# Kernel optimization log

Hardware: AMD Instinct MI355X
Metric: run time of the kernel (lower is better)

The kernel has to match this reference:

```python
import jax, jax.numpy as jnp
import numpy as np

H_IMG, W_IMG = 48, 64  # feature-map resolution hard-coded in the module
NUM_HEADS = 8


def get_positional_encodings(B, N, dtype=jnp.float32):
    # (p3^2, p4^2, p3*p4, p3, p4, 1) on normalized grid; intrinsics=None path
    ys = jnp.linspace(-1.0, 1.0, H_IMG, dtype=dtype)
    xs = jnp.linspace(-1.0, 1.0, W_IMG, dtype=dtype)
    p3 = jnp.tile(ys, W_IMG)           # [N] = ys repeated W times (torch repeat)
    p4 = jnp.repeat(xs, H_IMG)         # [N] = each x repeated H times
    pos = jnp.stack([p3 * p3, p4 * p4, p3 * p4, p3, p4, jnp.ones_like(p3)], axis=-1)  # [N,6]
    return jnp.broadcast_to(pos[None], (B, N, 6))


def setup_inputs() -> dict:
    key = jax.random.key(0)
    k1, k2, k3, k4, k5 = jax.random.split(key, 5)
    B, N, C = 2, H_IMG * W_IMG, 256
    s = 0.02
    return {
        "x1": jax.random.normal(k1, (B, N, C), jnp.float32),
        "x2": jax.random.normal(k2, (B, N, C), jnp.float32),
        "Wq": jax.random.normal(k3, (C, C), jnp.float32) * s,      # qkv (one-way: q only)
        "Wkv": jax.random.normal(k4, (C, 2 * C), jnp.float32) * s,  # qkv2 -> k,v
        "Wpf": jax.random.normal(k5, (C + 6 * NUM_HEADS, C), jnp.float32) * s,  # proj_fundamental
        "bpf": jnp.zeros((C,), jnp.float32),
    }


def reference(x1, x2, Wq, Wkv, Wpf, bpf):
    B, N, C = x1.shape
    H = NUM_HEADS
    d = C // H
    scale = d ** -0.5

    # q from x1; k,v from x2 (separate linear, matching torch reshape/permute split)
    q1 = (x1 @ Wq).reshape(B, N, H, d).transpose(0, 2, 1, 3)          # [B,H,N,d]
    kv = (x2 @ Wkv).reshape(B, N, 2, H, d)
    k2 = kv[:, :, 0].transpose(0, 2, 1, 3)                            # [B,H,N,d]
    v2 = kv[:, :, 1].transpose(0, 2, 1, 3)                            # [B,H,N,d]

    attn = jax.nn.softmax(jnp.einsum('bhnd,bhmd->bhnm', q1, k2) * scale, axis=-1)  # [B,H,N,N]

    pos = get_positional_encodings(B, N, x1.dtype)                    # [B,N,6]
    v2p = jnp.concatenate(
        [v2, jnp.broadcast_to(pos[:, None], (B, H, N, 6))], axis=-1)  # [B,H,N,d+6]

    y = jnp.einsum('bhnm,bhmd->bhnd', attn, v2p)                      # [B,H,N,d+6]
    y = y.transpose(0, 2, 1, 3).reshape(B, N, H * (d + 6))            # [B,N,C+6H]
    y = y @ Wpf + bpf                                                 # [B,N,C]
    y = y.reshape(B, N, H, d).transpose(0, 2, 1, 3)                   # [B,H,N,d]

    return jnp.concatenate([attn, y], axis=-1)                        # [B,H,N,N+d]
```

## Files before the change

### kernel.cpp

```cpp
#include <hip/hip_runtime.h>
#include <hip/hip_bf16.h>
#include <cstdint>
#include <cstddef>

#define NB 2
#define NH 8
#define BHN 16
#define NN 3072
#define CC 256
#define DD 32
#define OUTW 3104
#define VW 48
#define KP 384

typedef __attribute__((ext_vector_type(8))) __bf16 bf16x8;
typedef __attribute__((ext_vector_type(4))) short short4v;
typedef __attribute__((ext_vector_type(4))) float f32x4;

static __device__ __forceinline__ unsigned short f2bf(float f) {
    __hip_bfloat16 h = __float2bfloat16(f);
    return *reinterpret_cast<unsigned short*>(&h);
}

static __device__ __forceinline__ bf16x8 ldb8(const unsigned short* p) {
    return *(const bf16x8*)p;
}

static __device__ __forceinline__ f32x4 mfma16(bf16x8 a, bf16x8 b, f32x4 c) {
    return __builtin_amdgcn_mfma_f32_16x16x32_bf16(a, b, c, 0, 0, 0);
}

static __device__ __forceinline__ float bfhi2f(unsigned u) {
    union { unsigned u; float f; } v; v.u = u & 0xffff0000u; return v.f;
}
static __device__ __forceinline__ float bflo2f(unsigned u) {
    union { unsigned u; float f; } v; v.u = u << 16; return v.f;
}

__global__ __launch_bounds__(256) void prep_kernel(
    const float* __restrict__ x1, const float* __restrict__ x2,
    const float* __restrict__ Wq, const float* __restrict__ Wkv,
    const float* __restrict__ Wpf,
    unsigned short* __restrict__ x1b, unsigned short* __restrict__ x2b,
    unsigned short* __restrict__ Wt, unsigned short* __restrict__ Wpft,
    unsigned short* __restrict__ v2pT)
{
    int i = blockIdx.x * 256 + threadIdx.x;
    const int S_X = NB * NN * CC;
    if (i < S_X) { x1b[i] = f2bf(x1[i]); return; }
    i -= S_X;
    if (i < S_X) { x2b[i] = f2bf(x2[i]); return; }
    i -= S_X;
    const int S_WT = 768 * CC;
    if (i < S_WT) {
        int j = i >> 8, kk = i & 255;
        float w = (j < 256) ? Wq[kk * 256 + j] : Wkv[kk * 512 + (j - 256)];
        Wt[i] = f2bf(w);
        return;
    }
    i -= S_WT;
    const int S_WP = 256 * KP;
    if (i < S_WP) {
        int c2 = i / KP, t = i - c2 * KP;
        int h = t / VW, cc = t - h * VW;
        unsigned short v = 0;
        if (cc < 38) v = f2bf(Wpf[(h * 38 + cc) * 256 + c2]);
        Wpft[i] = v;
        return;
    }
    i -= S_WP;
    const int S_POS = BHN * 16 * NN;
    if (i < S_POS) {
        int n = i % NN;
        int r = i / NN;
        int bh = r >> 4;
        int c = (r & 15) + 32;
        float val = 0.f;
        if (c < 38) {
            float p3 = -1.f + 2.f * (float)(n % 48) / 47.f;
            float p4 = -1.f + 2.f * (float)(n / 48) / 63.f;
            float pv[6] = { p3 * p3, p4 * p4, p3 * p4, p3, p4, 1.f };
            val = pv[c - 32];
        }
        v2pT[((size_t)bh * VW + c) * NN + n] = f2bf(val);
    }
}

__global__ __launch_bounds__(256) void qkv_kernel(
    const unsigned short* __restrict__ x1b, const unsigned short* __restrict__ x2b,
    const unsigned short* __restrict__ Wt,
    unsigned short* __restrict__ qbh, unsigned short* __restrict__ kbh,
    unsigned short* __restrict__ v2pT)
{
    int rt = blockIdx.x, ct = blockIdx.y;
    int wv = threadIdx.x >> 6, lane = threadIdx.x & 63;
    int g = lane >> 4, q = lane & 15;
    int row0 = rt * 64 + wv * 16;
    const unsigned short* A = (ct < 4) ? x1b : x2b;
    const unsigned short* arow = A + (size_t)(row0 + q) * CC + g * 8;
    const unsigned short* brow = Wt + (size_t)(ct * 64 + q) * CC + g * 8;
    f32x4 acc[4];
    #pragma unroll
    for (int cb = 0; cb < 4; ++cb) acc[cb] = f32x4{0.f, 0.f, 0.f, 0.f};
    for (int k0 = 0; k0 < CC; k0 += 32) {
        bf16x8 af = ldb8(arow + k0);
        #pragma unroll
        for (int cb = 0; cb < 4; ++cb)
            acc[cb] = mfma16(af, ldb8(brow + (size_t)cb * 16 * CC + k0), acc[cb]);
    }
    int b = row0 / NN, nb = row0 % NN;
    #pragma unroll
    for (int cb = 0; cb < 4; ++cb) {
        int jj = ct * 64 + cb * 16 + q;
        #pragma unroll
        for (int r = 0; r < 4; ++r) {
            int n = nb + 4 * g + r;
            unsigned short bv = f2bf(acc[cb][r]);
            if (jj < 256) {
                int h = jj >> 5, c = jj & 31;
                qbh[(size_t)((b * NH + h) * NN + n) * DD + c] = bv;
            } else if (jj < 512) {
                int jk = jj - 256; int h = jk >> 5, c = jk & 31;
                kbh[(size_t)((b * NH + h) * NN + n) * DD + c] = bv;
            } else {
                int jv = jj - 512; int h = jv >> 5, c = jv & 31;
                v2pT[(size_t)((b * NH + h) * VW + c) * NN + n] = bv;
            }
        }
    }
}

__global__ __launch_bounds__(256) void attn_kernel(
    const unsigned short* __restrict__ qbh, const unsigned short* __restrict__ kbh,
    const unsigned short* __restrict__ v2pT,
    float* __restrict__ out, unsigned short* __restrict__ yacc)
{
    __shared__ unsigned short ptile[4][16][256];
    const float C = 0.17677669529663687f * 1.4426950408889634f;

    int id = blockIdx.x;
    int xcd = id & 7;
    int slot = id >> 3;
    int bh = xcd * 2 + (slot & 1);
    int qt = slot >> 1;

    int wv = threadIdx.x >> 6, lane = threadIdx.x & 63;
    int g = lane >> 4, q = lane & 15;
    int qrow = qt * 64 + wv * 16;

    bf16x8 qf = ldb8(qbh + (size_t)(bh * NN + qrow + q) * DD + g * 8);
    const unsigned short* kbase = kbh + (size_t)bh * NN * DD;
    const unsigned short* vbase = v2pT + (size_t)bh * VW * NN;

    float l = 0.f;
    {
        bf16x8 kf0 = ldb8(kbase + (size_t)(q) * DD + g * 8);
        bf16x8 kf1 = ldb8(kbase + (size_t)(16 + q) * DD + g * 8);
        for (int it = 0; it < 96; ++it) {
            int m0 = it * 32;
            bf16x8 kn0 = ldb8(kbase + (size_t)(m0 + 32 + q) * DD + g * 8);
            bf16x8 kn1 = ldb8(kbase + (size_t)(m0 + 48 + q) * DD + g * 8);
            f32x4 z = {0.f, 0.f, 0.f, 0.f};
            f32x4 s0 = mfma16(kf0, qf, z);
            f32x4 s1 = mfma16(kf1, qf, z);
            #pragma unroll
            for (int r = 0; r < 4; ++r)
                l += exp2f(s0[r] * C) + exp2f(s1[r] * C);
            kf0 = kn0; kf1 = kn1;
        }
    }
    l += __shfl_xor(l, 16, 64);
    l += __shfl_xor(l, 32, 64);
    float nl2 = -__log2f(l);

    f32x4 yt0 = {0.f,0.f,0.f,0.f}, yt1 = yt0, yt2 = yt0;
    char* myt = (char*)&ptile[wv][0][0];
    char* prow = myt + q * 512;
    unsigned swq = (unsigned)((q & 7) << 4);

    bf16x8 kf0 = ldb8(kbase + (size_t)(q) * DD + g * 8);
    bf16x8 kf1 = ldb8(kbase + (size_t)(16 + q) * DD + g * 8);
    bf16x8 vf0 = ldb8(vbase + (size_t)(q) * NN + g * 8);
    bf16x8 vf1 = ldb8(vbase + (size_t)(16 + q) * NN + g * 8);
    bf16x8 vf2 = ldb8(vbase + (size_t)(32 + q) * NN + g * 8);

    for (int ph = 0; ph < 12; ++ph) {
        #pragma unroll
        for (int it2 = 0; it2 < 8; ++it2) {
            int m0 = ph * 256 + it2 * 32;
            bf16x8 kn0 = ldb8(kbase + (size_t)(m0 + 32 + q) * DD + g * 8);
            bf16x8 kn1 = ldb8(kbase + (size_t)(m0 + 48 + q) * DD + g * 8);
            bf16x8 vn0 = ldb8(vbase + (size_t)(q) * NN + m0 + 32 + g * 8);
            bf16x8 vn1 = ldb8(vbase + (size_t)(16 + q) * NN + m0 + 32 + g * 8);
            bf16x8 vn2 = ldb8(vbase + (size_t)(32 + q) * NN + m0 + 32 + g * 8);

            f32x4 z = {0.f, 0.f, 0.f, 0.f};
            f32x4 s0 = mfma16(kf0, qf, z);
            f32x4 s1 = mfma16(kf1, qf, z);
            short4v pk0, pk1;
            #pragma unroll
            for (int r = 0; r < 4; ++r) {
                pk0[r] = (short)f2bf(exp2f(__builtin_fmaf(s0[r], C, nl2)));
                pk1[r] = (short)f2bf(exp2f(__builtin_fmaf(s1[r], C, nl2)));
            }
            unsigned b0 = (unsigned)(it2 * 64 + 8 * g);
            *(short4v*)(prow + (b0 ^ swq)) = pk0;
            *(short4v*)(prow + ((b0 + 32) ^ swq)) = pk1;
            asm volatile("s_waitcnt lgkmcnt(0)" ::: "memory");
            __builtin_amdgcn_sched_barrier(0);
            bf16x8 pf = *(const bf16x8*)(prow + ((unsigned)(it2 * 64 + 16 * g) ^ swq));
            yt0 = mfma16(vf0, pf, yt0);
            yt1 = mfma16(vf1, pf, yt1);
            yt2 = mfma16(vf2, pf, yt2);
            kf0 = kn0; kf1 = kn1; vf0 = vn0; vf1 = vn1; vf2 = vn2;
        }
        #pragma unroll
        for (int i = 0; i < 16; ++i) {
            unsigned off = ((unsigned)(lane * 8)) ^ ((unsigned)((i & 7) << 4));
            uint2 d = *(const uint2*)(myt + i * 512 + off);
            f32x4 v;
            v[0] = bflo2f(d.x); v[1] = bfhi2f(d.x);
            v[2] = bflo2f(d.y); v[3] = bfhi2f(d.y);
            float* dst = out + (size_t)(bh * NN + qrow + i) * OUTW + ph * 256 + lane * 4;
            *(f32x4*)dst = v;
        }
    }

    int b = bh >> 3, h = bh & 7;
    int nrow = qrow + q;
    unsigned short* yrow = yacc + (size_t)(b * NN + nrow) * KP + h * VW;
    f32x4 yts[3] = { yt0, yt1, yt2 };
    #pragma unroll
    for (int cb = 0; cb < 3; ++cb) {
        short4v pk;
        #pragma unroll
        for (int r = 0; r < 4; ++r) pk[r] = (short)f2bf(yts[cb][r]);
        *(short4v*)(yrow + cb * 16 + 4 * g) = pk;
    }
}

__global__ __launch_bounds__(256) void proj_kernel(
    const unsigned short* __restrict__ yacc, const unsigned short* __restrict__ Wpft,
    const float* __restrict__ bpf, float* __restrict__ out)
{
    int rt = blockIdx.x, ct = blockIdx.y;
    int wv = threadIdx.x >> 6, lane = threadIdx.x & 63;
    int g = lane >> 4, q = lane & 15;
    int row0 = rt * 64 + wv * 16;
    const unsigned short* arow = yacc + (size_t)(row0 + q) * KP + g * 8;
    const unsigned short* b0 = Wpft + (size_t)(ct * 64 + q) * KP + g * 8;
    f32x4 acc[4];
    #pragma unroll
    for (int cb = 0; cb < 4; ++cb) acc[cb] = f32x4{0.f, 0.f, 0.f, 0.f};
    for (int k0 = 0; k0 < KP; k0 += 32) {
        bf16x8 af = ldb8(arow + k0);
        #pragma unroll
        for (int cb = 0; cb < 4; ++cb)
            acc[cb] = mfma16(af, ldb8(b0 + (size_t)cb * 16 * KP + k0), acc[cb]);
    }
    int b = row0 / NN, nb = row0 % NN;
    #pragma unroll
    for (int cb = 0; cb < 4; ++cb) {
        int c2 = ct * 64 + cb * 16 + q;
        float bias = bpf[c2];
        int h = c2 >> 5, c = c2 & 31;
        float* obase = out + (size_t)((b * NH + h) * NN) * OUTW + NN + c;
        #pragma unroll
        for (int r = 0; r < 4; ++r) {
            int n = nb + 4 * g + r;
            __builtin_nontemporal_store(acc[cb][r] + bias, &obase[(size_t)n * OUTW]);
        }
    }
}

extern "C" void kernel_launch(void* const* d_in, const int* in_sizes, int n_in,
                              void* d_out, int out_size, void* d_ws, size_t ws_size,
                              hipStream_t stream)
{
    (void)in_sizes; (void)n_in; (void)out_size; (void)ws_size;
    const float* x1  = (const float*)d_in[0];
    const float* x2  = (const float*)d_in[1];
    const float* Wq  = (const float*)d_in[2];
    const float* Wkv = (const float*)d_in[3];
    const float* Wpf = (const float*)d_in[4];
    const float* bpf = (const float*)d_in[5];
    float* out = (float*)d_out;
    char* ws = (char*)d_ws;

    unsigned short* x1b  = (unsigned short*)(ws + 0);
    unsigned short* x2b  = (unsigned short*)(ws + 3145728);
    unsigned short* Wt   = (unsigned short*)(ws + 6291456);
    unsigned short* Wpft = (unsigned short*)(ws + 6684672);
    unsigned short* qbh  = (unsigned short*)(ws + 6881280);
    unsigned short* kbh  = (unsigned short*)(ws + 10027008);
    unsigned short* v2pT = (unsigned short*)(ws + 13172736);
    unsigned short* yacc = (unsigned short*)(ws + 17891328);

    prep_kernel<<<16512, 256, 0, stream>>>(x1, x2, Wq, Wkv, Wpf, x1b, x2b, Wt, Wpft, v2pT);
    qkv_kernel<<<dim3(96, 12), 256, 0, stream>>>(x1b, x2b, Wt, qbh, kbh, v2pT);
    attn_kernel<<<768, 256, 0, stream>>>(qbh, kbh, v2pT, out, yacc);
    proj_kernel<<<dim3(96, 4), 256, 0, stream>>>(yacc, Wpft, bpf, out);
}
```

Before: 285.3 us.

## Split attention key range across waves with shared 16-row query tile

Each block now handles 16 query rows, and its four waves split the key dimension (split-K) instead of each wave owning its own rows. The softmax denominator and the P·V partial sums are reduced across waves through shared memory. The block writes full 1024-wide attention row chunks with nontemporal stores. The grid grows fourfold to 3072 blocks. This gives more parallelism and coalesced, wider output writes, in exchange for extra barriers and the cross-wave reduction.

```diff
diff --git a/kernel.cpp b/kernel.cpp
--- a/kernel.cpp
+++ b/kernel.cpp
@@ -135,18 +135,19 @@
     const unsigned short* __restrict__ v2pT,
     float* __restrict__ out, unsigned short* __restrict__ yacc)
 {
-    __shared__ unsigned short ptile[4][16][256];
+    __shared__ unsigned short tile[16][1024];
+    __shared__ float lred[4][16];
     const float C = 0.17677669529663687f * 1.4426950408889634f;
 
     int id = blockIdx.x;
     int xcd = id & 7;
     int slot = id >> 3;
     int bh = xcd * 2 + (slot & 1);
-    int qt = slot >> 1;
+    int tl = slot >> 1;
+    int qrow = tl * 16;
 
     int wv = threadIdx.x >> 6, lane = threadIdx.x & 63;
     int g = lane >> 4, q = lane & 15;
-    int qrow = qt * 64 + wv * 16;
 
     bf16x8 qf = ldb8(qbh + (size_t)(bh * NN + qrow + q) * DD + g * 8);
     const unsigned short* kbase = kbh + (size_t)bh * NN * DD;
@@ -154,10 +155,11 @@
 
     float l = 0.f;
     {
-        bf16x8 kf0 = ldb8(kbase + (size_t)(q) * DD + g * 8);
-        bf16x8 kf1 = ldb8(kbase + (size_t)(16 + q) * DD + g * 8);
-        for (int it = 0; it < 96; ++it) {
-            int m0 = it * 32;
+        int mb = wv * 768;
+        bf16x8 kf0 = ldb8(kbase + (size_t)(mb + q) * DD + g * 8);
+        bf16x8 kf1 = ldb8(kbase + (size_t)(mb + 16 + q) * DD + g * 8);
+        for (int it = 0; it < 24; ++it) {
+            int m0 = mb + it * 32;
             bf16x8 kn0 = ldb8(kbase + (size_t)(m0 + 32 + q) * DD + g * 8);
             bf16x8 kn1 = ldb8(kbase + (size_t)(m0 + 48 + q) * DD + g * 8);
             f32x4 z = {0.f, 0.f, 0.f, 0.f};
@@ -171,28 +173,32 @@
     }
     l += __shfl_xor(l, 16, 64);
     l += __shfl_xor(l, 32, 64);
-    float nl2 = -__log2f(l);
+    if (lane < 16) lred[wv][q] = l;
+    __syncthreads();
+    float nl2 = -__log2f(lred[0][q] + lred[1][q] + lred[2][q] + lred[3][q]);
 
     f32x4 yt0 = {0.f,0.f,0.f,0.f}, yt1 = yt0, yt2 = yt0;
-    char* myt = (char*)&ptile[wv][0][0];
-    char* prow = myt + q * 512;
+    char* tbase = (char*)&tile[0][0];
+    char* prowc = tbase + q * 2048;
     unsigned swq = (unsigned)((q & 7) << 4);
-
-    bf16x8 kf0 = ldb8(kbase + (size_t)(q) * DD + g * 8);
-    bf16x8 kf1 = ldb8(kbase + (size_t)(16 + q) * DD + g * 8);
-    bf16x8 vf0 = ldb8(vbase + (size_t)(q) * NN + g * 8);
-    bf16x8 vf1 = ldb8(vbase + (size_t)(16 + q) * NN + g * 8);
-    bf16x8 vf2 = ldb8(vbase + (size_t)(32 + q) * NN + g * 8);
-
-    for (int ph = 0; ph < 12; ++ph) {
+    int wb = wv * 512;
+
+    for (int ph = 0; ph < 3; ++ph) {
+        int pbase = ph * 1024 + wv * 256;
+        bf16x8 kf0 = ldb8(kbase + (size_t)(pbase + q) * DD + g * 8);
+        bf16x8 kf1 = ldb8(kbase + (size_t)(pbase + 16 + q) * DD + g * 8);
+        bf16x8 vf0 = ldb8(vbase + (size_t)(q) * NN + pbase + g * 8);
+        bf16x8 vf1 = ldb8(vbase + (size_t)(16 + q) * NN + pbase + g * 8);
+        bf16x8 vf2 = ldb8(vbase + (size_t)(32 + q) * NN + pbase + g * 8);
         #pragma unroll
         for (int it2 = 0; it2 < 8; ++it2) {
-            int m0 = ph * 256 + it2 * 32;
-            bf16x8 kn0 = ldb8(kbase + (size_t)(m0 + 32 + q) * DD + g * 8);
-            bf16x8 kn1 = ldb8(kbase + (size_t)(m0 + 48 + q) * DD + g * 8);
-            bf16x8 vn0 = ldb8(vbase + (size_t)(q) * NN + m0 + 32 + g * 8);
-            bf16x8 vn1 = ldb8(vbase + (size_t)(16 + q) * NN + m0 + 32 + g * 8);
-            bf16x8 vn2 = ldb8(vbase + (size_t)(32 + q) * NN + m0 + 32 + g * 8);
+            int m0 = pbase + it2 * 32;
+            int mn = (it2 < 7) ? (m0 + 32) : ((ph + 1) * 1024 + wv * 256);
+            bf16x8 kn0 = ldb8(kbase + (size_t)(mn + q) * DD + g * 8);
+            bf16x8 kn1 = ldb8(kbase + (size_t)(mn + 16 + q) * DD + g * 8);
+            bf16x8 vn0 = ldb8(vbase + (size_t)(q) * NN + mn + g * 8);
+            bf16x8 vn1 = ldb8(vbase + (size_t)(16 + q) * NN + mn + g * 8);
+            bf16x8 vn2 = ldb8(vbase + (size_t)(32 + q) * NN + mn + g * 8);
 
             f32x4 z = {0.f, 0.f, 0.f, 0.f};
             f32x4 s0 = mfma16(kf0, qf, z);
@@ -203,39 +209,64 @@
                 pk0[r] = (short)f2bf(exp2f(__builtin_fmaf(s0[r], C, nl2)));
                 pk1[r] = (short)f2bf(exp2f(__builtin_fmaf(s1[r], C, nl2)));
             }
-            unsigned b0 = (unsigned)(it2 * 64 + 8 * g);
-            *(short4v*)(prow + (b0 ^ swq)) = pk0;
-            *(short4v*)(prow + ((b0 + 32) ^ swq)) = pk1;
+            unsigned b0 = (unsigned)(wb + it2 * 64 + 8 * g);
+            *(short4v*)(prowc + (b0 ^ swq)) = pk0;
+            *(short4v*)(prowc + ((b0 + 32) ^ swq)) = pk1;
             asm volatile("s_waitcnt lgkmcnt(0)" ::: "memory");
             __builtin_amdgcn_sched_barrier(0);
-            bf16x8 pf = *(const bf16x8*)(prow + ((unsigned)(it2 * 64 + 16 * g) ^ swq));
+            bf16x8 pf = *(const bf16x8*)(prowc + ((unsigned)(wb + it2 * 64 + 16 * g) ^ swq));
             yt0 = mfma16(vf0, pf, yt0);
             yt1 = mfma16(vf1, pf, yt1);
             yt2 = mfma16(vf2, pf, yt2);
             kf0 = kn0; kf1 = kn1; vf0 = vn0; vf1 = vn1; vf2 = vn2;
         }
-        #pragma unroll
-        for (int i = 0; i < 16; ++i) {
-            unsigned off = ((unsigned)(lane * 8)) ^ ((unsigned)((i & 7) << 4));
-            uint2 d = *(const uint2*)(myt + i * 512 + off);
-            f32x4 v;
-            v[0] = bflo2f(d.x); v[1] = bfhi2f(d.x);
-            v[2] = bflo2f(d.y); v[3] = bfhi2f(d.y);
-            float* dst = out + (size_t)(bh * NN + qrow + i) * OUTW + ph * 256 + lane * 4;
-            *(f32x4*)dst = v;
-        }
-    }
-
-    int b = bh >> 3, h = bh & 7;
-    int nrow = qrow + q;
-    unsigned short* yrow = yacc + (size_t)(b * NN + nrow) * KP + h * VW;
-    f32x4 yts[3] = { yt0, yt1, yt2 };
-    #pragma unroll
-    for (int cb = 0; cb < 3; ++cb) {
-        short4v pk;
-        #pragma unroll
-        for (int r = 0; r < 4; ++r) pk[r] = (short)f2bf(yts[cb][r]);
-        *(short4v*)(yrow + cb * 16 + 4 * g) = pk;
+        __syncthreads();
+        #pragma unroll
+        for (int j = 0; j < 4; ++j) {
+            int r = wv * 4 + j;
+            const char* rsrc = tbase + r * 2048;
+            unsigned swr = (unsigned)((r & 7) << 4);
+            float* dst = out + (size_t)(bh * NN + qrow + r) * OUTW + ph * 1024 + lane * 4;
+            #pragma unroll
+            for (int st = 0; st < 4; ++st) {
+                unsigned off = ((unsigned)(st * 512 + lane * 8)) ^ swr;
+                unsigned long long d = *(const unsigned long long*)(rsrc + off);
+                unsigned dlo = (unsigned)d, dhi = (unsigned)(d >> 32);
+                f32x4 v;
+                v[0] = bflo2f(dlo); v[1] = bfhi2f(dlo);
+                v[2] = bflo2f(dhi); v[3] = bfhi2f(dhi);
+                __builtin_nontemporal_store(v, (f32x4*)(dst + st * 256));
+            }
+        }
+        __syncthreads();
+    }
+
+    float* yl = (float*)tbase;
+    {
+        f32x4 yts[3] = { yt0, yt1, yt2 };
+        #pragma unroll
+        for (int cb = 0; cb < 3; ++cb)
+            #pragma unroll
+            for (int r = 0; r < 4; ++r)
+                yl[(wv * 48 + cb * 16 + 4 * g + r) * 17 + q] = yts[cb][r];
+    }
+    __syncthreads();
+    {
+        int t = threadIdx.x;
+        if (t < 192) {
+            int c0 = (t >> 4) << 2;
+            int qq = t & 15;
+            int b = bh >> 3, h = bh & 7;
+            short4v pk;
+            #pragma unroll
+            for (int rr = 0; rr < 4; ++rr) {
+                int c = c0 + rr;
+                float s = yl[(0 * 48 + c) * 17 + qq] + yl[(1 * 48 + c) * 17 + qq]
+                        + yl[(2 * 48 + c) * 17 + qq] + yl[(3 * 48 + c) * 17 + qq];
+                pk[rr] = (short)f2bf(s);
+            }
+            *(short4v*)(yacc + (size_t)(b * NN + qrow + qq) * KP + h * VW + c0) = pk;
+        }
     }
 }
 
@@ -298,6 +329,6 @@
 
     prep_kernel<<<16512, 256, 0, stream>>>(x1, x2, Wq, Wkv, Wpf, x1b, x2b, Wt, Wpft, v2pT);
     qkv_kernel<<<dim3(96, 12), 256, 0, stream>>>(x1b, x2b, Wt, qbh, kbh, v2pT);
-    attn_kernel<<<768, 256, 0, stream>>>(qbh, kbh, v2pT, out, yacc);
+    attn_kernel<<<3072, 256, 0, stream>>>(qbh, kbh, v2pT, out, yacc);
     proj_kernel<<<dim3(96, 4), 256, 0, stream>>>(yacc, Wpft, bpf, out);
 }
```

Measured after the change: 258.6 us. 1.1x faster.
